# Performance work log

Hardware: AMD Instinct MI355X
Metric: run time of the kernel (lower is better)

The kernel has to match this reference:

```python
import jax, jax.numpy as jnp
import numpy as np
from jax import lax

B_, L_, C_IN = 32, 1024, 3
D_MODEL, D_STATE, D_CONV, EXPAND = 256, 16, 4, 2
D_INNER = EXPAND * D_MODEL           # 512
DT_RANK = D_MODEL // 16              # 16
N_HEADS, N_CLASS = 8, 10
LN_EPS = 1e-5


def _pos_emb(L, d):
    pos = np.arange(L, dtype=np.float32)[:, None]
    div = np.exp(np.arange(0, d, 2, dtype=np.float32) * (-np.log(10000.0) / d))
    pe = np.zeros((L, d), np.float32)
    pe[:, 0::2] = np.sin(pos * div)
    pe[:, 1::2] = np.cos(pos * div)
    return jnp.asarray(pe)


def setup_inputs() -> dict:
    key = jax.random.key(0)
    ks = jax.random.split(key, 12)
    f = lambda k, shp, s: jax.random.normal(k, shp, jnp.float32) * s
    return {
        'x_enc': f(ks[0], (B_, L_, C_IN), 1.0),
        'x_mark_enc': jnp.ones((B_, L_), jnp.float32),
        'conv_emb_w': f(ks[1], (D_MODEL, C_IN, 3), (2.0 / (C_IN * 3)) ** 0.5),
        'in_proj_w': f(ks[2], (2 * D_INNER, D_MODEL), D_MODEL ** -0.5),
        'conv1d_w': f(ks[3], (D_INNER, 1, D_CONV), D_CONV ** -0.5),
        'conv1d_b': f(ks[4], (D_INNER,), 0.02),
        'x_proj_w': f(ks[5], (DT_RANK + 2 * D_STATE, D_INNER), D_INNER ** -0.5),
        'dt_proj_w': f(ks[6], (D_INNER, DT_RANK), DT_RANK ** -0.5),
        'dt_proj_b': f(ks[7], (D_INNER,), 0.1) - 2.0,
        'A_log': jnp.log(jnp.tile(jnp.arange(1, D_STATE + 1, dtype=jnp.float32), (D_INNER, 1))),
        'D': jnp.ones((D_INNER,), jnp.float32),
        'out_proj_w': f(ks[8], (D_MODEL, D_INNER), D_INNER ** -0.5),
        'ln_g': jnp.ones((D_MODEL,), jnp.float32),
        'ln_b': jnp.zeros((D_MODEL,), jnp.float32),
        'out_w': f(ks[9], (N_CLASS, D_MODEL), D_MODEL ** -0.5),
        'attn_w': f(ks[10], (N_HEADS, D_MODEL), 0.02),
        'attn_b': jnp.ones((N_HEADS,), jnp.float32),
    }


def _forward(x_enc, x_mark_enc, conv_emb_w, in_proj_w, conv1d_w, conv1d_b,
             x_proj_w, dt_proj_w, dt_proj_b, A_log, D, out_proj_w,
             ln_g, ln_b, out_w, attn_w, attn_b):
    silu = jax.nn.silu
    # --- embedding: Conv1d 'same' with replicate padding + sinusoidal PE ---
    xp = jnp.pad(x_enc, ((0, 0), (1, 1), (0, 0)), mode='edge')      # k=3 -> pad (1,1)
    x = lax.conv_general_dilated(xp.transpose(0, 2, 1), conv_emb_w, (1,), 'VALID',
                                 dimension_numbers=('NCH', 'OIH', 'NCH')).transpose(0, 2, 1)
    x = x + _pos_emb(L_, D_MODEL)[None]                              # (B,L,D)

    # --- Mamba_TimeVariant (standard Mamba selective scan) ---
    xz = jnp.einsum('bld,ed->ble', x, in_proj_w)                     # (B,L,2*Din)
    xin, z = xz[..., :D_INNER], xz[..., D_INNER:]
    # depthwise causal conv, kernel D_CONV
    xc = jnp.pad(xin.transpose(0, 2, 1), ((0, 0), (0, 0), (D_CONV - 1, 0)))
    xc = lax.conv_general_dilated(xc, conv1d_w, (1,), 'VALID',
                                  feature_group_count=D_INNER,
                                  dimension_numbers=('NCH', 'OIH', 'NCH'))
    xc = silu(xc.transpose(0, 2, 1) + conv1d_b)                      # (B,L,Din)

    dbl = jnp.einsum('bld,ed->ble', xc, x_proj_w)                    # (B,L,dt_rank+2*N)
    dtr = dbl[..., :DT_RANK]
    Bm = dbl[..., DT_RANK:DT_RANK + D_STATE]                         # (B,L,N)
    Cm = dbl[..., DT_RANK + D_STATE:]                                # (B,L,N)
    dt = jax.nn.softplus(jnp.einsum('blr,dr->bld', dtr, dt_proj_w) + dt_proj_b)
    A = -jnp.exp(A_log)                                              # (Din,N)

    def step(h, inp):
        dt_t, B_t, C_t, x_t = inp                                    # (B,Din),(B,N),(B,N),(B,Din)
        dA = jnp.exp(dt_t[..., None] * A)                            # (B,Din,N)
        h = dA * h + dt_t[..., None] * B_t[:, None, :] * x_t[..., None]
        y = jnp.einsum('bdn,bn->bd', h, C_t)
        return h, y

    h0 = jnp.zeros((B_, D_INNER, D_STATE), xc.dtype)
    inputs = (dt.transpose(1, 0, 2), Bm.transpose(1, 0, 2),
              Cm.transpose(1, 0, 2), xc.transpose(1, 0, 2))
    _, ys = lax.scan(step, h0, inputs)                               # (L,B,Din)
    y = ys.transpose(1, 0, 2) + xc * D                               # skip via D
    y = y * silu(z)
    m = jnp.einsum('bld,ed->ble', y, out_proj_w)                     # (B,L,Dmodel)

    # LayerNorm + SiLU
    mu = m.mean(-1, keepdims=True)
    var = ((m - mu) ** 2).mean(-1, keepdims=True)
    m = (m - mu) * lax.rsqrt(var + LN_EPS) * ln_g + ln_b
    m = silu(m)

    # classification head
    logit = jnp.einsum('bld,cd->blc', m, out_w) * x_mark_enc[..., None]
    s = jnp.einsum('bld,hd->blh', m, attn_w) + attn_b                # (B,L,H)
    w = jax.nn.softmax(jnp.max(s, axis=2, keepdims=True), axis=1)    # (B,L,1)
    return (logit * w).sum(1)                                        # (B,num_class)


def reference(x_enc, x_mark_enc, conv_emb_w, in_proj_w, conv1d_w, conv1d_b,
              x_proj_w, dt_proj_w, dt_proj_b, A_log, D, out_proj_w,
              ln_g, ln_b, out_w, attn_w, attn_b):
    return _forward(x_enc, x_mark_enc, conv_emb_w, in_proj_w, conv1d_w, conv1d_b,
                    x_proj_w, dt_proj_w, dt_proj_b, A_log, D, out_proj_w,
                    ln_g, ln_b, out_w, attn_w, attn_b)
```

## Files before the change

kernel.cpp:

```cpp
#include <hip/hip_runtime.h>
#include <hip/hip_bf16.h>
#include <math.h>

#define B_  32
#define L_  1024
#define CIN 3
#define DM  256
#define DI  512
#define NST 16
#define NH  8
#define NC  10
#define M_TOT (B_*L_)

typedef unsigned short u16;
typedef __attribute__((ext_vector_type(8))) short bf16x8;
typedef __attribute__((ext_vector_type(4))) float f32x4;
typedef const __attribute__((address_space(1))) unsigned int* gptr_t;
typedef __attribute__((address_space(3))) unsigned int* sptr_t;

static __device__ __forceinline__ float sigmoidf_(float x) {
    return 1.0f / (1.0f + __expf(-x));
}
static __device__ __forceinline__ u16 f2bf(float f) {
    unsigned int u = __float_as_uint(f);
    return (u16)((u + 0x7FFF + ((u >> 16) & 1)) >> 16);
}
static __device__ __forceinline__ float bf2f(u16 u) {
    return __uint_as_float(((unsigned int)u) << 16);
}
static __device__ __forceinline__ float2 bf2x2(unsigned int u) {
    return make_float2(bf2f((u16)(u & 0xffff)), bf2f((u16)(u >> 16)));
}
static __device__ __forceinline__ void gload_lds16(const void* g, void* s) {
    __builtin_amdgcn_global_load_lds(
        (gptr_t)(unsigned long long)g,
        (sptr_t)(unsigned int)(unsigned long long)s, 16, 0, 0);
}

static __device__ __forceinline__ void reduce8_pair(float& a, float& b) {
    asm volatile(
        "s_nop 1\n\t"
        "v_add_f32 %0, %0, %0 quad_perm:[1,0,3,2] row_mask:0xf bank_mask:0xf\n\t"
        "v_add_f32 %1, %1, %1 quad_perm:[1,0,3,2] row_mask:0xf bank_mask:0xf\n\t"
        "s_nop 1\n\t"
        "v_add_f32 %0, %0, %0 quad_perm:[2,3,0,1] row_mask:0xf bank_mask:0xf\n\t"
        "v_add_f32 %1, %1, %1 quad_perm:[2,3,0,1] row_mask:0xf bank_mask:0xf\n\t"
        "s_nop 1\n\t"
        "v_add_f32 %0, %0, %0 row_half_mirror row_mask:0xf bank_mask:0xf\n\t"
        "v_add_f32 %1, %1, %1 row_half_mirror row_mask:0xf bank_mask:0xf\n\t"
        "s_nop 1\n\t"
        : "+v"(a), "+v"(b));
}

__global__ __launch_bounds__(256) void k_cvt2(const float* __restrict__ wi,
        const float* __restrict__ wo, u16* __restrict__ obi,
        u16* __restrict__ obo) {
    int idx = blockIdx.x * 256 + threadIdx.x;
    const float* src;
    u16* dst;
    int i;
    if (idx < (2*DI*DM)/4) { src = wi; dst = obi; i = idx*4; }
    else { src = wo; dst = obo; i = (idx - (2*DI*DM)/4)*4; }
    float4 v = *(const float4*)(src + i);
    ushort4 o;
    o.x = f2bf(v.x); o.y = f2bf(v.y); o.z = f2bf(v.z); o.w = f2bf(v.w);
    *(ushort4*)(dst + i) = o;
}

__global__ __launch_bounds__(256) void k_embed(const float* __restrict__ xe,
        const float* __restrict__ w, u16* __restrict__ x) {
    int bl = blockIdx.x;
    int l = bl & (L_-1);
    int b = bl >> 10;
    int d = threadIdx.x;
    const float* xb = xe + (size_t)b * L_ * CIN;
    int t0 = l > 0 ? l-1 : 0;
    int t2 = l < L_-1 ? l+1 : L_-1;
    const float* w3 = w + d*9;
    float acc = 0.f;
    #pragma unroll
    for (int i = 0; i < 3; ++i) {
        acc += xb[t0*3+i] * w3[i*3+0];
        acc += xb[l *3+i] * w3[i*3+1];
        acc += xb[t2*3+i] * w3[i*3+2];
    }
    int j = d >> 1;
    float div = expf((float)(2*j) * (-logf(10000.0f)/(float)DM));
    float ang = (float)l * div;
    acc += (d & 1) ? cosf(ang) : sinf(ang);
    x[(size_t)bl*DM + d] = f2bf(acc);
}

#define BKK 32
__global__ __launch_bounds__(256) void k_gemm_mfma(
        const u16* __restrict__ A, const u16* __restrict__ W,
        float* __restrict__ O1f, u16* __restrict__ O1b,
        u16* __restrict__ O2b, int M, int N, int K, int S) {
    __shared__ u16 As[128*BKK];
    __shared__ u16 Bs[128*BKK];
    int tid = threadIdx.x;
    int row0 = blockIdx.y * 128, col0 = blockIdx.x * 128;
    int wave = tid >> 6, lane = tid & 63;
    int wr = (wave >> 1) * 64, wc = (wave & 1) * 64;
    int l16 = lane & 15, kl = lane >> 4;
    int sr_ = lane >> 2;
    int sc_ = lane & 3;

    f32x4 acc[4][4];
    #pragma unroll
    for (int m = 0; m < 4; ++m)
        #pragma unroll
        for (int n = 0; n < 4; ++n)
            acc[m][n] = (f32x4){0.f, 0.f, 0.f, 0.f};

    for (int k0 = 0; k0 < K; k0 += BKK) {
        __syncthreads();
        #pragma unroll
        for (int t = 0; t < 2; ++t) {
            int r = wave*32 + t*16 + sr_;
            int csw = sc_ ^ ((r >> 2) & 3);
            gload_lds16(A + (size_t)(row0 + r)*K + k0 + csw*8,
                        &As[(wave*32 + t*16)*BKK]);
            gload_lds16(W + (size_t)(col0 + r)*K + k0 + csw*8,
                        &Bs[(wave*32 + t*16)*BKK]);
        }
        __syncthreads();
        bf16x8 af[4], bf[4];
        #pragma unroll
        for (int m = 0; m < 4; ++m) {
            int row = wr + m*16 + l16;
            af[m] = *(const bf16x8*)&As[row*BKK + (kl ^ ((row>>2)&3))*8];
        }
        #pragma unroll
        for (int n = 0; n < 4; ++n) {
            int row = wc + n*16 + l16;
            bf[n] = *(const bf16x8*)&Bs[row*BKK + (kl ^ ((row>>2)&3))*8];
        }
        #pragma unroll
        for (int m = 0; m < 4; ++m)
            #pragma unroll
            for (int n = 0; n < 4; ++n)
                acc[m][n] = __builtin_amdgcn_mfma_f32_16x16x32_bf16(
                                af[m], bf[n], acc[m][n], 0, 0, 0);
    }

    #pragma unroll
    for (int m = 0; m < 4; ++m) {
        int rbase = row0 + wr + m*16 + kl*4;
        #pragma unroll
        for (int n = 0; n < 4; ++n) {
            int col = col0 + wc + n*16 + l16;
            #pragma unroll
            for (int r = 0; r < 4; ++r) {
                float v = acc[m][n][r];
                if (col < S) {
                    if (O1b) O1b[(size_t)(rbase + r)*S + col] = f2bf(v);
                    else     O1f[(size_t)(rbase + r)*S + col] = v;
                } else {
                    O2b[(size_t)(rbase + r)*(N - S) + (col - S)] = f2bf(v);
                }
            }
        }
    }
}

__global__ __launch_bounds__(256) void k_conv(const u16* __restrict__ xin,
        const float* __restrict__ w, const float* __restrict__ bias,
        u16* __restrict__ xc) {
    size_t i4 = (size_t)blockIdx.x * 256 + threadIdx.x;
    int d4 = (int)(i4 & (DI/4 - 1)) * 4;
    size_t m = i4 >> 7;
    int l = (int)(m & (L_-1));
    float4 wv0 = *(const float4*)(w + (size_t)(d4+0)*4);
    float4 wv1 = *(const float4*)(w + (size_t)(d4+1)*4);
    float4 wv2 = *(const float4*)(w + (size_t)(d4+2)*4);
    float4 wv3 = *(const float4*)(w + (size_t)(d4+3)*4);
    float W[4][4] = {{wv0.x,wv0.y,wv0.z,wv0.w},{wv1.x,wv1.y,wv1.z,wv1.w},
                     {wv2.x,wv2.y,wv2.z,wv2.w},{wv3.x,wv3.y,wv3.z,wv3.w}};
    float4 acc = *(const float4*)(bias + d4);
    #pragma unroll
    for (int k = 0; k < 4; ++k) {
        int t = l + k - 3;
        if (t >= 0) {
            ushort4 xv = *(const ushort4*)(xin + (m + k - 3)*DI + d4);
            acc.x = fmaf(bf2f(xv.x), W[0][k], acc.x);
            acc.y = fmaf(bf2f(xv.y), W[1][k], acc.y);
            acc.z = fmaf(bf2f(xv.z), W[2][k], acc.z);
            acc.w = fmaf(bf2f(xv.w), W[3][k], acc.w);
        }
    }
    ushort4 r;
    r.x = f2bf(acc.x * sigmoidf_(acc.x));
    r.y = f2bf(acc.y * sigmoidf_(acc.y));
    r.z = f2bf(acc.z * sigmoidf_(acc.z));
    r.w = f2bf(acc.w * sigmoidf_(acc.w));
    *(ushort4*)(xc + m*DI + d4) = r;
}

#define XBM 128
#define XBK 16
__global__ __launch_bounds__(256) void k_xproj(const u16* __restrict__ xc,
        const float* __restrict__ wp, float* __restrict__ dbl) {
    __shared__ float As[XBK][XBM];
    __shared__ float Ws[XBK][48];
    int tid = threadIdx.x;
    int row0 = blockIdx.x * XBM;
    int lr = tid >> 1;
    int lk = (tid & 1) * 8;
    int we = tid >> 2;
    int wk = (tid & 3) * 4;
    int tx = tid & 15;
    int ty = tid >> 4;
    float acc[8][3];
    #pragma unroll
    for (int i = 0; i < 8; ++i)
        #pragma unroll
        for (int j = 0; j < 3; ++j) acc[i][j] = 0.f;

    for (int k0 = 0; k0 < DI; k0 += XBK) {
        ushort4 ab0 = *(const ushort4*)(xc + (size_t)(row0+lr)*DI + k0 + lk);
        ushort4 ab1 = *(const ushort4*)(xc + (size_t)(row0+lr)*DI + k0 + lk + 4);
        float4 w0 = make_float4(0.f,0.f,0.f,0.f);
        if (tid < 192) w0 = *(const float4*)(wp + (size_t)we*DI + k0 + wk);
        __syncthreads();
        As[lk+0][lr]=bf2f(ab0.x); As[lk+1][lr]=bf2f(ab0.y);
        As[lk+2][lr]=bf2f(ab0.z); As[lk+3][lr]=bf2f(ab0.w);
        As[lk+4][lr]=bf2f(ab1.x); As[lk+5][lr]=bf2f(ab1.y);
        As[lk+6][lr]=bf2f(ab1.z); As[lk+7][lr]=bf2f(ab1.w);
        if (tid < 192) {
            Ws[wk+0][we]=w0.x; Ws[wk+1][we]=w0.y; Ws[wk+2][we]=w0.z; Ws[wk+3][we]=w0.w;
        }
        __syncthreads();
        #pragma unroll
        for (int k = 0; k < XBK; ++k) {
            float4 av0 = *(const float4*)&As[k][ty*8];
            float4 av1 = *(const float4*)&As[k][ty*8+4];
            float w0_ = Ws[k][tx*3+0];
            float w1_ = Ws[k][tx*3+1];
            float w2_ = Ws[k][tx*3+2];
            float ar[8] = {av0.x,av0.y,av0.z,av0.w,av1.x,av1.y,av1.z,av1.w};
            #pragma unroll
            for (int i = 0; i < 8; ++i) {
                acc[i][0] = fmaf(ar[i], w0_, acc[i][0]);
                acc[i][1] = fmaf(ar[i], w1_, acc[i][1]);
                acc[i][2] = fmaf(ar[i], w2_, acc[i][2]);
            }
        }
    }
    #pragma unroll
    for (int i = 0; i < 8; ++i) {
        size_t r = row0 + ty*8 + i;
        #pragma unroll
        for (int j = 0; j < 3; ++j)
            dbl[r*48 + tx*3 + j] = acc[i][j];
    }
}

__global__ __launch_bounds__(256) void k_dtproj(const float* __restrict__ dbl,
        const float* __restrict__ dtw, const float* __restrict__ dtb,
        u16* __restrict__ dt) {
    __shared__ float wl[DI][17];
    __shared__ float rl[32][16];
    size_t m0 = (size_t)blockIdx.x * 32;
    for (int i = threadIdx.x; i < DI*16; i += 256)
        wl[i >> 4][i & 15] = dtw[i];
    for (int i = threadIdx.x; i < 32*16; i += 256)
        rl[i >> 4][i & 15] = dbl[(m0 + (i>>4))*48 + (i & 15)];
    __syncthreads();
    float b0 = dtb[threadIdx.x];
    float b1 = dtb[256 + threadIdx.x];
    for (int mm = 0; mm < 32; ++mm) {
        #pragma unroll
        for (int half = 0; half < 2; ++half) {
            int d = half*256 + threadIdx.x;
            float acc = half ? b1 : b0;
            #pragma unroll
            for (int r = 0; r < 16; ++r)
                acc = fmaf(rl[mm][r], wl[d][r], acc);
            float sp = fmaxf(acc, 0.f) + log1pf(__expf(-fabsf(acc)));
            dt[(m0+mm)*DI + d] = f2bf(sp);
        }
    }
}

#define SCAN_T 64
__global__ __launch_bounds__(256) void k_scan(const u16* __restrict__ dt,
        const u16* __restrict__ xcb, const float* __restrict__ dbl,
        const float* __restrict__ A_log, const float* __restrict__ Dp,
        const u16* __restrict__ zbf, u16* __restrict__ ybf) {
    __shared__ float4 sq4[SCAN_T*33];
    __shared__ float2 sBC2[SCAN_T*18];

    int tid = threadIdx.x;
    int wave = tid >> 6, lane = tid & 63;
    int chw = lane >> 3;
    int j   = lane & 7;
    int ch  = wave*8 + chw;
    int d0 = blockIdx.x * 32;
    int b  = blockIdx.y;
    int d  = d0 + ch;
    float Aa = -expf(A_log[(size_t)d*NST + 2*j])     * 1.44269504f;
    float Ab = -expf(A_log[(size_t)d*NST + 2*j + 1]) * 1.44269504f;
    float h0 = 0.f, h1 = 0.f;
    size_t base = (size_t)b * L_;

    int st = tid >> 2;
    int sc = (tid & 3) * 8;
    int ns = (tid & 3) * 4;
    float4 Dva = *(const float4*)(Dp + d0 + sc);
    float4 Dvb = *(const float4*)(Dp + d0 + sc + 4);

    for (int t0 = 0; t0 < L_; t0 += SCAN_T) {
        __syncthreads();
        {
            size_t row = base + t0 + st;
            uint4 dv = *(const uint4*)(dt  + row*DI + d0 + sc);
            uint4 xv = *(const uint4*)(xcb + row*DI + d0 + sc);
            uint4 zv = *(const uint4*)(zbf + row*DI + d0 + sc);
            float4 Bv = *(const float4*)(dbl + row*48 + 16 + ns);
            float4 Cv = *(const float4*)(dbl + row*48 + 32 + ns);
            float2 dt01 = bf2x2(dv.x), dt23 = bf2x2(dv.y);
            float2 dt45 = bf2x2(dv.z), dt67 = bf2x2(dv.w);
            float2 x01 = bf2x2(xv.x), x23 = bf2x2(xv.y);
            float2 x45 = bf2x2(xv.z), x67 = bf2x2(xv.w);
            float2 z01 = bf2x2(zv.x), z23 = bf2x2(zv.y);
            float2 z45 = bf2x2(zv.z), z67 = bf2x2(zv.w);
            float dtr[8] = { dt01.x, dt01.y, dt23.x, dt23.y,
                             dt45.x, dt45.y, dt67.x, dt67.y };
            float xr[8]  = { x01.x, x01.y, x23.x, x23.y,
                             x45.x, x45.y, x67.x, x67.y };
            float zr[8]  = { z01.x, z01.y, z23.x, z23.y,
                             z45.x, z45.y, z67.x, z67.y };
            float Dr[8] = { Dva.x, Dva.y, Dva.z, Dva.w,
                            Dvb.x, Dvb.y, Dvb.z, Dvb.w };
            #pragma unroll
            for (int k = 0; k < 8; ++k) {
                float g = zr[k] * sigmoidf_(zr[k]);
                sq4[st*33 + sc + k] = make_float4(dtr[k], dtr[k]*xr[k],
                                                  xr[k]*Dr[k]*g, g);
            }
            *(float4*)&sBC2[st*18 + ns]     = make_float4(Bv.x, Cv.x, Bv.y, Cv.y);
            *(float4*)&sBC2[st*18 + ns + 2] = make_float4(Bv.z, Cv.z, Bv.w, Cv.w);
        }
        __syncthreads();

        #pragma unroll 2
        for (int t2 = 0; t2 < SCAN_T/2; ++t2) {
            float4 bc0 = *(const float4*)&sBC2[(2*t2)*18 + 2*j];
            float4 bc1 = *(const float4*)&sBC2[(2*t2+1)*18 + 2*j];
            float4 q0 = sq4[(2*t2)*33 + ch];
            float4 q1 = sq4[(2*t2+1)*33 + ch];
            float dA0 = exp2f(q0.x * Aa);
            float dA1 = exp2f(q0.x * Ab);
            h0 = fmaf(dA0, h0, q0.y * bc0.x);
            h1 = fmaf(dA1, h1, q0.y * bc0.z);
            float p0 = fmaf(h1, bc0.w, h0 * bc0.y);
            dA0 = exp2f(q1.x * Aa);
            dA1 = exp2f(q1.x * Ab);
            h0 = fmaf(dA0, h0, q1.y * bc1.x);
            h1 = fmaf(dA1, h1, q1.y * bc1.z);
            float p1 = fmaf(h1, bc1.w, h0 * bc1.y);
            reduce8_pair(p0, p1);
            if (j == 0) {
                size_t row = base + t0 + 2*t2;
                ybf[row*DI + d]     = f2bf(fmaf(p0, q0.w, q0.z));
                ybf[(row+1)*DI + d] = f2bf(fmaf(p1, q1.w, q1.z));
            }
        }
    }
}

#define HBK 32
__global__ __launch_bounds__(256) void k_lnheads18(const u16* __restrict__ mb,
        const float* __restrict__ g, const float* __restrict__ bta,
        const float* __restrict__ aw, const float* __restrict__ ow,
        float* __restrict__ r18) {
    __shared__ float As[128][36];
    __shared__ float Ws[18][36];
    __shared__ float gb[DM], bb[DM];
    int tid = threadIdx.x;
    int row0 = blockIdx.x * 128;
    int sr = tid >> 1, sk = (tid & 1) * 16;
    gb[tid] = g[tid];
    bb[tid] = bta[tid];
    const u16* mrow = mb + (size_t)(row0 + sr)*DM;

    float s1 = 0.f, s2 = 0.f;
    for (int k0 = 0; k0 < DM; k0 += HBK) {
        uint4 va = *(const uint4*)(mrow + k0 + sk);
        uint4 vb = *(const uint4*)(mrow + k0 + sk + 8);
        unsigned int ua[8] = {va.x, va.y, va.z, va.w, vb.x, vb.y, vb.z, vb.w};
        #pragma unroll
        for (int q = 0; q < 8; ++q) {
            float2 p = bf2x2(ua[q]);
            s1 += p.x + p.y;
            s2 += p.x*p.x + p.y*p.y;
        }
    }
    s1 += __shfl_xor(s1, 1);
    s2 += __shfl_xor(s2, 1);
    float mu = s1 * (1.0f/DM);
    float var = fmaxf(s2 * (1.0f/DM) - mu*mu, 0.f);
    float rstd = 1.0f / sqrtf(var + 1e-5f);

    int r = tid >> 1, cb = (tid & 1) * 9;
    float acc[9];
    #pragma unroll
    for (int c = 0; c < 9; ++c) acc[c] = 0.f;

    for (int k0 = 0; k0 < DM; k0 += HBK) {
        uint4 va = *(const uint4*)(mrow + k0 + sk);
        uint4 vb = *(const uint4*)(mrow + k0 + sk + 8);
        float4 wv = make_float4(0.f,0.f,0.f,0.f);
        int wc = tid >> 3, wk = (tid & 7) * 4;
        if (tid < 144) {
            const float* wsrc = (wc < NH) ? (aw + wc*DM) : (ow + (wc-NH)*DM);
            wv = *(const float4*)(wsrc + k0 + wk);
        }
        __syncthreads();
        {
            unsigned int ua[8] = {va.x, va.y, va.z, va.w, vb.x, vb.y, vb.z, vb.w};
            #pragma unroll
            for (int q = 0; q < 8; ++q) {
                float2 p = bf2x2(ua[q]);
                int c0 = k0 + sk + 2*q;
                float o0 = (p.x - mu)*rstd*gb[c0]   + bb[c0];
                float o1 = (p.y - mu)*rstd*gb[c0+1] + bb[c0+1];
                As[sr][sk + 2*q]     = o0 * sigmoidf_(o0);
                As[sr][sk + 2*q + 1] = o1 * sigmoidf_(o1);
            }
            if (tid < 144)
                *(float4*)&Ws[wc][wk] = wv;
        }
        __syncthreads();
        #pragma unroll
        for (int k4 = 0; k4 < HBK/4; ++k4) {
            float4 av = *(const float4*)&As[r][k4*4];
            #pragma unroll
            for (int c = 0; c < 9; ++c) {
                float4 w4 = *(const float4*)&Ws[cb + c][k4*4];
                acc[c] += av.x*w4.x + av.y*w4.y + av.z*w4.z + av.w*w4.w;
            }
        }
    }
    #pragma unroll
    for (int c = 0; c < 9; ++c)
        r18[(size_t)(row0 + r)*18 + cb + c] = acc[c];
}

__global__ __launch_bounds__(256) void k_final(const float* __restrict__ r18,
        const float* __restrict__ ab, const float* __restrict__ xmark,
        float* __restrict__ out) {
    __shared__ float e[L_];
    __shared__ float red[256];
    int b = blockIdx.x;
    int tid = threadIdx.x;
    float abr[NH];
    #pragma unroll
    for (int j = 0; j < NH; ++j) abr[j] = ab[j];
    float mx = -1e30f;
    for (int l = tid; l < L_; l += 256) {
        const float* rr = r18 + ((size_t)b*L_ + l)*18;
        float sm = rr[0] + abr[0];
        #pragma unroll
        for (int j = 1; j < NH; ++j) sm = fmaxf(sm, rr[j] + abr[j]);
        e[l] = sm;
        mx = fmaxf(mx, sm);
    }
    #pragma unroll
    for (int o = 32; o > 0; o >>= 1) mx = fmaxf(mx, __shfl_xor(mx, o));
    red[tid] = mx;
    __syncthreads();
    mx = fmaxf(fmaxf(red[0], red[64]), fmaxf(red[128], red[192]));
    __syncthreads();
    float ssum = 0.f;
    for (int l = tid; l < L_; l += 256) {
        float ev = __expf(e[l] - mx);
        e[l] = ev;
        ssum += ev;
    }
    #pragma unroll
    for (int o = 32; o > 0; o >>= 1) ssum += __shfl_xor(ssum, o);
    if ((tid & 63) == 0) red[tid >> 6] = ssum;
    __syncthreads();
    float inv = 1.0f / (red[0]+red[1]+red[2]+red[3]);
    float acc[NC];
    #pragma unroll
    for (int c = 0; c < NC; ++c) acc[c] = 0.f;
    for (int l = tid; l < L_; l += 256) {
        float wl = e[l] * xmark[(size_t)b*L_ + l];
        const float* lg = r18 + ((size_t)b*L_ + l)*18 + NH;
        #pragma unroll
        for (int c = 0; c < NC; ++c) acc[c] = fmaf(wl, lg[c], acc[c]);
    }
    __syncthreads();
    for (int c = 0; c < NC; ++c) {
        red[tid] = acc[c];
        __syncthreads();
        if (tid < 64) {
            float s2 = red[tid]+red[tid+64]+red[tid+128]+red[tid+192];
            #pragma unroll
            for (int o = 32; o > 0; o >>= 1) s2 += __shfl_xor(s2, o);
            if (tid == 0) out[(size_t)b*NC + c] = s2 * inv;
        }
        __syncthreads();
    }
}

extern "C" void kernel_launch(void* const* d_in, const int* in_sizes, int n_in,
                              void* d_out, int out_size, void* d_ws, size_t ws_size,
                              hipStream_t stream) {
    const float* x_enc  = (const float*)d_in[0];
    const float* x_mark = (const float*)d_in[1];
    const float* cemb_w = (const float*)d_in[2];
    const float* inp_w  = (const float*)d_in[3];
    const float* c1_w   = (const float*)d_in[4];
    const float* c1_b   = (const float*)d_in[5];
    const float* xp_w   = (const float*)d_in[6];
    const float* dtp_w  = (const float*)d_in[7];
    const float* dtp_b  = (const float*)d_in[8];
    const float* A_log  = (const float*)d_in[9];
    const float* Dp     = (const float*)d_in[10];
    const float* outp_w = (const float*)d_in[11];
    const float* ln_g   = (const float*)d_in[12];
    const float* ln_b   = (const float*)d_in[13];
    const float* out_w  = (const float*)d_in[14];
    const float* attn_w = (const float*)d_in[15];
    const float* attn_b = (const float*)d_in[16];
    float* out = (float*)d_out;

    char* ws = (char*)d_ws;
    size_t o = 0;
    u16*   xbf  = (u16*)(ws + o);   o += (size_t)M_TOT*DM*2;
    u16*   xinb = (u16*)(ws + o);   o += (size_t)M_TOT*DI*2;
    u16*   zbf  = (u16*)(ws + o);   o += (size_t)M_TOT*DI*2;
    u16*   xcb  = (u16*)(ws + o);   o += (size_t)M_TOT*DI*2;
    u16*   ybf  = (u16*)(ws + o);   o += (size_t)M_TOT*DI*2;
    u16*   dt16 = (u16*)(ws + o);   o += (size_t)M_TOT*DI*2;
    u16*   mm16 = (u16*)(ws + o);   o += (size_t)M_TOT*DM*2;
    float* dbl  = (float*)(ws + o); o += (size_t)M_TOT*48*4;
    u16*   wbfi = (u16*)(ws + o);   o += (size_t)2*DI*DM*2;
    u16*   wbfo = (u16*)(ws + o);   o += (size_t)DM*DI*2;
    float* r18  = (float*)(ws + o); o += (size_t)M_TOT*18*4;

    k_cvt2  <<<(2*DI*DM + DM*DI)/1024, 256, 0, stream>>>(inp_w, outp_w,
                                                         wbfi, wbfo);
    k_embed <<<M_TOT, 256, 0, stream>>>(x_enc, cemb_w, xbf);
    k_gemm_mfma<<<dim3(8, M_TOT/128), 256, 0, stream>>>(xbf, wbfi,
                                nullptr, xinb, zbf, M_TOT, 2*DI, DM, DI);
    k_conv  <<<(M_TOT*DI/4)/256, 256, 0, stream>>>(xinb, c1_w, c1_b, xcb);
    k_xproj <<<M_TOT/XBM, 256, 0, stream>>>(xcb, xp_w, dbl);
    k_dtproj<<<M_TOT/32, 256, 0, stream>>>(dbl, dtp_w, dtp_b, dt16);
    k_scan  <<<dim3(DI/32, B_), 256, 0, stream>>>(dt16, xcb, dbl, A_log, Dp,
                                                  zbf, ybf);
    k_gemm_mfma<<<dim3(2, M_TOT/128), 256, 0, stream>>>(ybf, wbfo,
                                nullptr, mm16, zbf, M_TOT, DM, DI, DM);
    k_lnheads18<<<M_TOT/128, 256, 0, stream>>>(mm16, ln_g, ln_b, attn_w,
                                               out_w, r18);
    k_final <<<B_, 256, 0, stream>>>(r18, attn_b, x_mark, out);
}
```

Before: 436.5 us.

## Split selective scan into segments with carry-propagation pass

The sequential scan over L is split into 8 time segments. A pre-pass computes each segment's decay product and local state, a small fix-up kernel propagates carries across segments, and the main scan restarts each segment from its corrected initial state. This raises the grid from 512 blocks to 4096, so the serial per-block time loop is eight times shorter and more of the GPU is occupied. The cost is an extra read of dt, x and B, the extra exp work in the pre-pass, and two more launches.

```diff
diff --git a/kernel.cpp b/kernel.cpp
--- a/kernel.cpp
+++ b/kernel.cpp
@@ -11,6 +11,8 @@
 #define NH  8
 #define NC  10
 #define M_TOT (B_*L_)
+#define NSEG 8
+#define SEGT (L_/NSEG)
 
 typedef unsigned short u16;
 typedef __attribute__((ext_vector_type(8))) short bf16x8;
@@ -284,12 +286,12 @@
 }
 
 #define SCAN_T 64
-__global__ __launch_bounds__(256) void k_scan(const u16* __restrict__ dt,
+__global__ __launch_bounds__(256) void k_scanpre(const u16* __restrict__ dt,
         const u16* __restrict__ xcb, const float* __restrict__ dbl,
-        const float* __restrict__ A_log, const float* __restrict__ Dp,
-        const u16* __restrict__ zbf, u16* __restrict__ ybf) {
-    __shared__ float4 sq4[SCAN_T*33];
-    __shared__ float2 sBC2[SCAN_T*18];
+        const float* __restrict__ A_log,
+        float* __restrict__ aseg, float* __restrict__ hseg) {
+    __shared__ float2 sq2[SCAN_T*33];
+    __shared__ float2 sBp[SCAN_T*9];
 
     int tid = threadIdx.x;
     int wave = tid >> 6, lane = tid & 63;
@@ -298,10 +300,93 @@
     int ch  = wave*8 + chw;
     int d0 = blockIdx.x * 32;
     int b  = blockIdx.y;
+    int s  = blockIdx.z;
     int d  = d0 + ch;
     float Aa = -expf(A_log[(size_t)d*NST + 2*j])     * 1.44269504f;
     float Ab = -expf(A_log[(size_t)d*NST + 2*j + 1]) * 1.44269504f;
-    float h0 = 0.f, h1 = 0.f;
+    float h0 = 0.f, h1 = 0.f, ap0 = 1.f, ap1 = 1.f;
+    size_t base = (size_t)b * L_;
+
+    int st = tid >> 2;
+    int sc = (tid & 3) * 8;
+    int ns = (tid & 3) * 4;
+
+    for (int t0 = s*SEGT; t0 < (s+1)*SEGT; t0 += SCAN_T) {
+        __syncthreads();
+        {
+            size_t row = base + t0 + st;
+            uint4 dv = *(const uint4*)(dt  + row*DI + d0 + sc);
+            uint4 xv = *(const uint4*)(xcb + row*DI + d0 + sc);
+            float4 Bv = *(const float4*)(dbl + row*48 + 16 + ns);
+            float2 dt01 = bf2x2(dv.x), dt23 = bf2x2(dv.y);
+            float2 dt45 = bf2x2(dv.z), dt67 = bf2x2(dv.w);
+            float2 x01 = bf2x2(xv.x), x23 = bf2x2(xv.y);
+            float2 x45 = bf2x2(xv.z), x67 = bf2x2(xv.w);
+            float dtr[8] = { dt01.x, dt01.y, dt23.x, dt23.y,
+                             dt45.x, dt45.y, dt67.x, dt67.y };
+            float xr[8]  = { x01.x, x01.y, x23.x, x23.y,
+                             x45.x, x45.y, x67.x, x67.y };
+            #pragma unroll
+            for (int k = 0; k < 8; ++k)
+                sq2[st*33 + sc + k] = make_float2(dtr[k], dtr[k]*xr[k]);
+            sBp[st*9 + ns/2]     = make_float2(Bv.x, Bv.y);
+            sBp[st*9 + ns/2 + 1] = make_float2(Bv.z, Bv.w);
+        }
+        __syncthreads();
+
+        #pragma unroll 4
+        for (int t = 0; t < SCAN_T; ++t) {
+            float2 q  = sq2[t*33 + ch];
+            float2 Bp = sBp[t*9 + j];
+            float dA0 = exp2f(q.x * Aa);
+            float dA1 = exp2f(q.x * Ab);
+            ap0 *= dA0;
+            ap1 *= dA1;
+            h0 = fmaf(dA0, h0, q.y * Bp.x);
+            h1 = fmaf(dA1, h1, q.y * Bp.y);
+        }
+    }
+    size_t oidx = ((((size_t)s*B_ + b)*DI + d)*NST) + 2*j;
+    *(float2*)&aseg[oidx] = make_float2(ap0, ap1);
+    *(float2*)&hseg[oidx] = make_float2(h0, h1);
+}
+
+__global__ __launch_bounds__(256) void k_scanfix(const float* __restrict__ aseg,
+        float* __restrict__ hseg) {
+    size_t i = (size_t)blockIdx.x*256 + threadIdx.x;
+    size_t stride = (size_t)B_*DI*NST;
+    float hi = 0.f;
+    #pragma unroll
+    for (int s = 0; s < NSEG; ++s) {
+        float a  = aseg[s*stride + i];
+        float hf = hseg[s*stride + i];
+        hseg[s*stride + i] = hi;
+        hi = fmaf(a, hi, hf);
+    }
+}
+
+__global__ __launch_bounds__(256) void k_scan(const u16* __restrict__ dt,
+        const u16* __restrict__ xcb, const float* __restrict__ dbl,
+        const float* __restrict__ A_log, const float* __restrict__ Dp,
+        const u16* __restrict__ zbf, const float* __restrict__ hseg,
+        u16* __restrict__ ybf) {
+    __shared__ float4 sq4[SCAN_T*33];
+    __shared__ float2 sBC2[SCAN_T*18];
+
+    int tid = threadIdx.x;
+    int wave = tid >> 6, lane = tid & 63;
+    int chw = lane >> 3;
+    int j   = lane & 7;
+    int ch  = wave*8 + chw;
+    int d0 = blockIdx.x * 32;
+    int b  = blockIdx.y;
+    int s  = blockIdx.z;
+    int d  = d0 + ch;
+    float Aa = -expf(A_log[(size_t)d*NST + 2*j])     * 1.44269504f;
+    float Ab = -expf(A_log[(size_t)d*NST + 2*j + 1]) * 1.44269504f;
+    size_t oidx = ((((size_t)s*B_ + b)*DI + d)*NST) + 2*j;
+    float2 hi = *(const float2*)&hseg[oidx];
+    float h0 = hi.x, h1 = hi.y;
     size_t base = (size_t)b * L_;
 
     int st = tid >> 2;
@@ -310,7 +395,7 @@
     float4 Dva = *(const float4*)(Dp + d0 + sc);
     float4 Dvb = *(const float4*)(Dp + d0 + sc + 4);
 
-    for (int t0 = 0; t0 < L_; t0 += SCAN_T) {
+    for (int t0 = s*SEGT; t0 < (s+1)*SEGT; t0 += SCAN_T) {
         __syncthreads();
         {
             size_t row = base + t0 + st;
@@ -542,6 +627,8 @@
     u16*   wbfi = (u16*)(ws + o);   o += (size_t)2*DI*DM*2;
     u16*   wbfo = (u16*)(ws + o);   o += (size_t)DM*DI*2;
     float* r18  = (float*)(ws + o); o += (size_t)M_TOT*18*4;
+    float* aseg = (float*)(ws + o); o += (size_t)NSEG*B_*DI*NST*4;
+    float* hseg = (float*)(ws + o); o += (size_t)NSEG*B_*DI*NST*4;
 
     k_cvt2  <<<(2*DI*DM + DM*DI)/1024, 256, 0, stream>>>(inp_w, outp_w,
                                                          wbfi, wbfo);
@@ -551,8 +638,11 @@
     k_conv  <<<(M_TOT*DI/4)/256, 256, 0, stream>>>(xinb, c1_w, c1_b, xcb);
     k_xproj <<<M_TOT/XBM, 256, 0, stream>>>(xcb, xp_w, dbl);
     k_dtproj<<<M_TOT/32, 256, 0, stream>>>(dbl, dtp_w, dtp_b, dt16);
-    k_scan  <<<dim3(DI/32, B_), 256, 0, stream>>>(dt16, xcb, dbl, A_log, Dp,
-                                                  zbf, ybf);
+    k_scanpre<<<dim3(DI/32, B_, NSEG), 256, 0, stream>>>(dt16, xcb, dbl,
+                                                         A_log, aseg, hseg);
+    k_scanfix<<<(B_*DI*NST)/256, 256, 0, stream>>>(aseg, hseg);
+    k_scan  <<<dim3(DI/32, B_, NSEG), 256, 0, stream>>>(dt16, xcb, dbl, A_log,
+                                                 Dp, zbf, hseg, ybf);
     k_gemm_mfma<<<dim3(2, M_TOT/128), 256, 0, stream>>>(ybf, wbfo,
                                 nullptr, mm16, zbf, M_TOT, DM, DI, DM);
     k_lnheads18<<<M_TOT/128, 256, 0, stream>>>(mm16, ln_g, ln_b, attn_w,
```

Result: slower. 475.3 us (+8.9%).
